# Performance work log

Measured on AMD Instinct MI355X. Metric: run time of the kernel, lower is better.

The kernel has to match this reference:

```python
import jax, jax.numpy as jnp
import numpy as np

H = 128
N_USER, N_PC, N_URL = 100000, 20000, 50000
E_UP, E_UU = 250000, 500000
NUM_LAYERS = 2


def _sage(x_src, x_dst, src_idx, dst_idx, n_dst, Wl, bl, Wr):
    # PyG SAGEConv (aggr='mean', root_weight=True, lin_r bias=False):
    # out = lin_l(mean_j x_src[j]) + lin_r(x_dst)
    msg = x_src[src_idx]                                   # [E, H] gather
    agg = jax.ops.segment_sum(msg, dst_idx, num_segments=n_dst)
    cnt = jax.ops.segment_sum(jnp.ones((src_idx.shape[0], 1), x_src.dtype),
                              dst_idx, num_segments=n_dst)
    mean = agg / jnp.maximum(cnt, 1.0)
    return mean @ Wl + bl + x_dst @ Wr


def setup_inputs() -> dict:
    key = jax.random.key(0)
    ks = jax.random.split(key, 24)
    s = 0.05
    inp = {
        'x_user': jax.random.normal(ks[0], (N_USER, 6), jnp.float32),
        'x_pc': jax.random.normal(ks[1], (N_PC, 4), jnp.float32),
        'x_url': jax.random.normal(ks[2], (N_URL, 3), jnp.float32),
        'edge_up_src': jax.random.randint(ks[3], (E_UP,), 0, N_USER, jnp.int32),
        'edge_up_dst': jax.random.randint(ks[4], (E_UP,), 0, N_PC, jnp.int32),
        'edge_uu_src': jax.random.randint(ks[5], (E_UU,), 0, N_USER, jnp.int32),
        'edge_uu_dst': jax.random.randint(ks[6], (E_UU,), 0, N_URL, jnp.int32),
        # input projections
        'Wu': jax.random.normal(ks[7], (6, H), jnp.float32) * s,
        'bu': jnp.zeros((H,), jnp.float32),
        'Wp': jax.random.normal(ks[8], (4, H), jnp.float32) * s,
        'bp': jnp.zeros((H,), jnp.float32),
        'Wr_feat': jax.random.normal(ks[9], (3, H), jnp.float32) * s,
        'br_feat': jnp.zeros((H,), jnp.float32),
        # SAGEConv params, stacked over layers [L, H, H]
        'Wl_pc': jax.random.normal(ks[10], (NUM_LAYERS, H, H), jnp.float32) * s,
        'bl_pc': jnp.zeros((NUM_LAYERS, H), jnp.float32),
        'Wr_pc': jax.random.normal(ks[11], (NUM_LAYERS, H, H), jnp.float32) * s,
        'Wl_url': jax.random.normal(ks[12], (NUM_LAYERS, H, H), jnp.float32) * s,
        'bl_url': jnp.zeros((NUM_LAYERS, H), jnp.float32),
        'Wr_url': jax.random.normal(ks[13], (NUM_LAYERS, H, H), jnp.float32) * s,
        # context aggregation + classifier
        'Wctx': jax.random.normal(ks[14], (3 * H, H), jnp.float32) * s,
        'bctx': jnp.zeros((H,), jnp.float32),
        'Wc1': jax.random.normal(ks[15], (H, H // 2), jnp.float32) * s,
        'bc1': jnp.zeros((H // 2,), jnp.float32),
        'Wc2': jax.random.normal(ks[16], (H // 2, 2), jnp.float32) * s,
        'bc2': jnp.zeros((2,), jnp.float32),
    }
    return inp


def reference(x_user, x_pc, x_url,
              edge_up_src, edge_up_dst, edge_uu_src, edge_uu_dst,
              Wu, bu, Wp, bp, Wr_feat, br_feat,
              Wl_pc, bl_pc, Wr_pc, Wl_url, bl_url, Wr_url,
              Wctx, bctx, Wc1, bc1, Wc2, bc2):
    user = x_user @ Wu + bu          # [N_USER, H] (never updated by convs)
    pc = x_pc @ Wp + bp              # [N_PC, H]
    url = x_url @ Wr_feat + br_feat  # [N_URL, H]

    for i in range(NUM_LAYERS):
        pc_new = _sage(user, pc, edge_up_src, edge_up_dst, pc.shape[0],
                       Wl_pc[i], bl_pc[i], Wr_pc[i])
        url_new = _sage(user, url, edge_uu_src, edge_uu_dst, url.shape[0],
                        Wl_url[i], bl_url[i], Wr_url[i])
        if i == 0:
            pc = jax.nn.relu(pc_new)
            url = jax.nn.relu(url_new)
        else:
            pc = jax.nn.relu(pc_new + pc)
            url = jax.nn.relu(url_new + url)

    # aggregate_resource_context: scatter-add of resource embeddings into users
    pc_ctx = jax.ops.segment_sum(pc[edge_up_dst], edge_up_src, num_segments=user.shape[0])
    url_ctx = jax.ops.segment_sum(url[edge_uu_dst], edge_uu_src, num_segments=user.shape[0])
    combined = jnp.concatenate([user, pc_ctx, url_ctx], axis=1)   # [N_USER, 3H]
    enriched = combined @ Wctx + bctx

    # classifier (dropout inactive at inference)
    h = jax.nn.relu(enriched @ Wc1 + bc1)
    return h @ Wc2 + bc2
```

## Files before the change

kernel.cpp:

```cpp
#include <hip/hip_runtime.h>

typedef unsigned short u16;
typedef short short8_t __attribute__((ext_vector_type(8)));
typedef float floatx4 __attribute__((ext_vector_type(4)));

static constexpr int N_USER_C = 100000;
static constexpr int N_PC_C   = 20000;
static constexpr int N_URL_C  = 50000;
static constexpr int E_UP_C   = 250000;
static constexpr int E_UU_C   = 500000;

static constexpr int S_UPD = 48;
static constexpr int S_UUD = 40;
static constexpr int S_SRC = 24;

__device__ __forceinline__ float bf2f(u16 h) {
    return __uint_as_float(((unsigned)h) << 16);
}
__device__ __forceinline__ u16 f2bf(float f) {
    unsigned u = __float_as_uint(f);
    u += 0x7fffu + ((u >> 16) & 1u);
    return (u16)(u >> 16);
}

struct WcvtArgs { const float* src[12]; int n[12]; };

__global__ __launch_bounds__(256) void wcvt_kernel(WcvtArgs args, u16* __restrict__ dst)
{
    int idx = blockIdx.x * 256 + threadIdx.x;
    int m = idx >> 14, e = idx & 16383;
    int n = e >> 7, k = e & 127;
    int Nm = args.n[m];
    u16 v = 0;
    if (n < Nm) v = f2bf(args.src[m][k * Nm + n]);
    dst[(size_t)m * 16384 + n * 128 + k] = v;
}

struct Proj3Args {
    const float *Xu, *Wu, *bu, *Xp, *Wp, *bp, *Xr, *Wr, *br;
    u16 *ou, *op, *orr;
};
__global__ __launch_bounds__(256) void proj3_kernel(Proj3Args a)
{
    int idx = blockIdx.x * 256 + threadIdx.x;
    const float* X; const float* W; const float* b; u16* o; int K;
    if (idx < 1600000)       { X = a.Xu; W = a.Wu; b = a.bu; o = a.ou; K = 6; }
    else if (idx < 1920000)  { idx -= 1600000; X = a.Xp; W = a.Wp; b = a.bp; o = a.op; K = 4; }
    else                     { idx -= 1920000; X = a.Xr; W = a.Wr; b = a.br; o = a.orr; K = 3; }
    int r = idx >> 4, c0 = (idx & 15) * 8;
    float acc[8];
    {
        const float4 b0 = *(const float4*)(b + c0);
        const float4 b1 = *(const float4*)(b + c0 + 4);
        acc[0] = b0.x; acc[1] = b0.y; acc[2] = b0.z; acc[3] = b0.w;
        acc[4] = b1.x; acc[5] = b1.y; acc[6] = b1.z; acc[7] = b1.w;
    }
    for (int k = 0; k < K; ++k) {
        float xk = X[(size_t)r * K + k];
        const float4 w0 = *(const float4*)(W + k * 128 + c0);
        const float4 w1 = *(const float4*)(W + k * 128 + c0 + 4);
        acc[0] += xk * w0.x; acc[1] += xk * w0.y; acc[2] += xk * w0.z; acc[3] += xk * w0.w;
        acc[4] += xk * w1.x; acc[5] += xk * w1.y; acc[6] += xk * w1.z; acc[7] += xk * w1.w;
    }
    uint4 pk;
    pk.x = (unsigned)f2bf(acc[0]) | ((unsigned)f2bf(acc[1]) << 16);
    pk.y = (unsigned)f2bf(acc[2]) | ((unsigned)f2bf(acc[3]) << 16);
    pk.z = (unsigned)f2bf(acc[4]) | ((unsigned)f2bf(acc[5]) << 16);
    pk.w = (unsigned)f2bf(acc[6]) | ((unsigned)f2bf(acc[7]) << 16);
    *(uint4*)(o + (size_t)r * 128 + c0) = pk;
}

__global__ __launch_bounds__(256) void fill_all_kernel(
    const int* __restrict__ up_src, const int* __restrict__ up_dst,
    const int* __restrict__ uu_src, const int* __restrict__ uu_dst,
    int* __restrict__ cnt_up_dst, int* __restrict__ val_up_dst,
    int* __restrict__ cnt_up_src, u16* __restrict__ val_up_src,
    int* __restrict__ cnt_uu_dst, int* __restrict__ val_uu_dst,
    int* __restrict__ cnt_uu_src, u16* __restrict__ val_uu_src)
{
    const int range = blockIdx.x & 7;
    const int ebase = (blockIdx.x >> 3) * 2048 + threadIdx.x;
#pragma unroll
    for (int i = 0; i < 8; ++i) {
        int e = ebase + i * 256;
        if (e < E_UP_C) {
            int s = up_src[e], d = up_dst[e];
            if (d / 2500 == range) {
                int p = atomicAdd(&cnt_up_dst[d], 1);
                if (p < S_UPD) val_up_dst[d * S_UPD + p] = s;
            }
            if (s / 12500 == range) {
                int p = atomicAdd(&cnt_up_src[s], 1);
                if (p < S_SRC) val_up_src[s * S_SRC + p] = (u16)d;
            }
        }
        if (e < E_UU_C) {
            int s = uu_src[e], d = uu_dst[e];
            if (d / 6250 == range) {
                int p = atomicAdd(&cnt_uu_dst[d], 1);
                if (p < S_UUD) val_uu_dst[d * S_UUD + p] = s;
            }
            if (s / 12500 == range) {
                int p = atomicAdd(&cnt_uu_src[s], 1);
                if (p < S_SRC) val_uu_src[s * S_SRC + p] = (u16)d;
            }
        }
    }
}

__device__ __forceinline__ void gm_row(
    const u16* __restrict__ feat, const int* __restrict__ cnt,
    const int* __restrict__ vals, int stride, u16* __restrict__ outp, int row, int lane)
{
    int deg = cnt[row];
    deg = __builtin_amdgcn_readfirstlane(deg);
    int n = deg < stride ? deg : stride;
    const int* vp = vals + row * stride;
    float a0 = 0.f, a1 = 0.f, b0 = 0.f, b1 = 0.f;
    float c0 = 0.f, c1 = 0.f, d0 = 0.f, d1 = 0.f;
    int j = 0;
    for (; j + 4 <= n; j += 4) {
        int i0 = vp[j], i1 = vp[j + 1], i2 = vp[j + 2], i3 = vp[j + 3];
        unsigned u0 = *(const unsigned*)(feat + (size_t)i0 * 128 + lane * 2);
        unsigned u1 = *(const unsigned*)(feat + (size_t)i1 * 128 + lane * 2);
        unsigned u2 = *(const unsigned*)(feat + (size_t)i2 * 128 + lane * 2);
        unsigned u3 = *(const unsigned*)(feat + (size_t)i3 * 128 + lane * 2);
        a0 += bf2f((u16)(u0 & 0xffff)); a1 += bf2f((u16)(u0 >> 16));
        b0 += bf2f((u16)(u1 & 0xffff)); b1 += bf2f((u16)(u1 >> 16));
        c0 += bf2f((u16)(u2 & 0xffff)); c1 += bf2f((u16)(u2 >> 16));
        d0 += bf2f((u16)(u3 & 0xffff)); d1 += bf2f((u16)(u3 >> 16));
    }
    for (; j < n; ++j) {
        int i0 = vp[j];
        unsigned u0 = *(const unsigned*)(feat + (size_t)i0 * 128 + lane * 2);
        a0 += bf2f((u16)(u0 & 0xffff)); a1 += bf2f((u16)(u0 >> 16));
    }
    float ax = (a0 + b0) + (c0 + d0), ay = (a1 + b1) + (c1 + d1);
    float inv = 1.0f / fmaxf((float)deg, 1.0f);
    unsigned o = (unsigned)f2bf(ax * inv) | ((unsigned)f2bf(ay * inv) << 16);
    *(unsigned*)(outp + (size_t)row * 128 + lane * 2) = o;
}

__global__ __launch_bounds__(256) void gather_mean2_kernel(
    const u16* __restrict__ feat,
    const int* __restrict__ cnt_pc, const int* __restrict__ val_pc, u16* __restrict__ out_pc,
    const int* __restrict__ cnt_url, const int* __restrict__ val_url, u16* __restrict__ out_url)
{
    int b = blockIdx.x;
    int lane = threadIdx.x & 63, w = threadIdx.x >> 6;
    if (b < 5000) gm_row(feat, cnt_pc, val_pc, S_UPD, out_pc, b * 4 + w, lane);
    else          gm_row(feat, cnt_url, val_url, S_UUD, out_url, (b - 5000) * 4 + w, lane);
}

__device__ __forceinline__ unsigned ctx_ld(int t, int n0, const u16* __restrict__ vu,
    const u16* __restrict__ vr,
    const u16* __restrict__ pcW, const u16* __restrict__ urlW, int lane)
{
    bool isup = t < n0;
    const u16* vp = isup ? (vu + t) : (vr + (t - n0));
    int idx = *vp;
    const u16* base = isup ? pcW : urlW;
    return *(const unsigned*)(base + (size_t)idx * 128 + lane * 2);
}

__global__ __launch_bounds__(256) void ctx_gather_kernel(
    u16* __restrict__ enr,
    const int* __restrict__ cnt_up, const u16* __restrict__ val_up, const u16* __restrict__ pcW,
    const int* __restrict__ cnt_uu, const u16* __restrict__ val_uu, const u16* __restrict__ urlW,
    int M)
{
    int row = blockIdx.x * 4 + (threadIdx.x >> 6);
    if (row >= M) return;
    int lane = threadIdx.x & 63;
    int n0 = cnt_up[row], n1 = cnt_uu[row];
    n0 = __builtin_amdgcn_readfirstlane(n0); n1 = __builtin_amdgcn_readfirstlane(n1);
    n0 = n0 < S_SRC ? n0 : S_SRC; n1 = n1 < S_SRC ? n1 : S_SRC;
    int total = n0 + n1;
    const u16* vu = val_up + row * S_SRC;
    const u16* vr = val_uu + row * S_SRC;

    unsigned eu = *(const unsigned*)(enr + (size_t)row * 128 + lane * 2);
    float a0 = bf2f((u16)(eu & 0xffff)), a1 = bf2f((u16)(eu >> 16));
    float b0 = 0.f, b1 = 0.f, c0 = 0.f, c1 = 0.f, d0 = 0.f, d1 = 0.f;

    int t = 0;
    for (; t + 4 <= total; t += 4) {
        unsigned u0 = ctx_ld(t + 0, n0, vu, vr, pcW, urlW, lane);
        unsigned u1 = ctx_ld(t + 1, n0, vu, vr, pcW, urlW, lane);
        unsigned u2 = ctx_ld(t + 2, n0, vu, vr, pcW, urlW, lane);
        unsigned u3 = ctx_ld(t + 3, n0, vu, vr, pcW, urlW, lane);
        a0 += bf2f((u16)(u0 & 0xffff)); a1 += bf2f((u16)(u0 >> 16));
        b0 += bf2f((u16)(u1 & 0xffff)); b1 += bf2f((u16)(u1 >> 16));
        c0 += bf2f((u16)(u2 & 0xffff)); c1 += bf2f((u16)(u2 >> 16));
        d0 += bf2f((u16)(u3 & 0xffff)); d1 += bf2f((u16)(u3 >> 16));
    }
    for (; t < total; ++t) {
        unsigned u0 = ctx_ld(t, n0, vu, vr, pcW, urlW, lane);
        a0 += bf2f((u16)(u0 & 0xffff)); a1 += bf2f((u16)(u0 >> 16));
    }
    float ax = (a0 + b0) + (c0 + d0), ay = (a1 + b1) + (c1 + d1);
    unsigned o = (unsigned)f2bf(ax) | ((unsigned)f2bf(ay) << 16);
    *(unsigned*)(enr + (size_t)row * 128 + lane * 2) = o;
}

struct GSeg { const u16* A1; const u16* Wt1; const u16* A2; const u16* Wt2;
              const float* bias; u16* out; int M; int bstart; };
template<int NSEG> struct GArgs { GSeg s[NSEG]; };

template<int NT, bool HAS2, bool RES, bool RELU, int NSEG>
__global__ __launch_bounds__(256) void gemm_multi_kernel(GArgs<NSEG> ga)
{
    constexpr int ROWS = NT * 16;
    constexpr int PER_ROW = 256 / ROWS;
    constexpr int CHUNK = 32 / PER_ROW;
    constexpr int NC = HAS2 ? 8 : 4;

    __shared__ u16 Ws[ROWS * 40];

    int si = 0;
#pragma unroll
    for (int i = 1; i < NSEG; ++i) if ((int)blockIdx.x >= ga.s[i].bstart) si = i;
    const u16* A1 = ga.s[si].A1;  const u16* Wt1 = ga.s[si].Wt1;
    const u16* A2 = ga.s[si].A2;  const u16* Wt2 = ga.s[si].Wt2;
    const float* bias = ga.s[si].bias;
    u16* out = ga.s[si].out;
    const int M = ga.s[si].M;
    const int bb = blockIdx.x - ga.s[si].bstart;

    const int tid = threadIdx.x;
    const int wave = tid >> 6, lane = tid & 63;
    const int m = lane & 15, kq = lane >> 4;
    const int rbase = bb * 128 + wave * 32;
    const int sn = tid / PER_ROW, spart = tid % PER_ROW;

    floatx4 acc[2][NT];
#pragma unroll
    for (int mt = 0; mt < 2; ++mt)
#pragma unroll
        for (int nt = 0; nt < NT; ++nt) acc[mt][nt] = (floatx4)0.0f;

    short8_t a_next[2];
#pragma unroll
    for (int mt = 0; mt < 2; ++mt) {
        int row = rbase + mt * 16 + m; row = row < M ? row : M - 1;
        a_next[mt] = *(const short8_t*)(A1 + (size_t)row * 128 + kq * 8);
    }

    for (int c = 0; c < NC; ++c) {
        const int kc = (HAS2 ? (c & 3) : c) * 32;
        const u16* Wt = (HAS2 && (c >> 2)) ? Wt2 : Wt1;
        __syncthreads();
#pragma unroll
        for (int j = 0; j < CHUNK / 8; ++j) {
            short8_t v = *(const short8_t*)(Wt + (size_t)sn * 128 + kc + spart * CHUNK + j * 8);
            *(short8_t*)&Ws[sn * 40 + spart * CHUNK + j * 8] = v;
        }
        short8_t a_cur[2] = { a_next[0], a_next[1] };
        __syncthreads();
        if (c + 1 < NC) {
            int c1 = c + 1;
            int kc1 = (HAS2 ? (c1 & 3) : c1) * 32;
            const u16* Ap = (HAS2 && (c1 >> 2)) ? A2 : A1;
#pragma unroll
            for (int mt = 0; mt < 2; ++mt) {
                int row = rbase + mt * 16 + m; row = row < M ? row : M - 1;
                a_next[mt] = *(const short8_t*)(Ap + (size_t)row * 128 + kc1 + kq * 8);
            }
        }
#pragma unroll
        for (int nt = 0; nt < NT; ++nt) {
            short8_t b = *(const short8_t*)&Ws[(nt * 16 + m) * 40 + kq * 8];
            acc[0][nt] = __builtin_amdgcn_mfma_f32_16x16x32_bf16(a_cur[0], b, acc[0][nt], 0, 0, 0);
            acc[1][nt] = __builtin_amdgcn_mfma_f32_16x16x32_bf16(a_cur[1], b, acc[1][nt], 0, 0, 0);
        }
    }

#pragma unroll
    for (int nt = 0; nt < NT; ++nt) {
        int col = nt * 16 + m;
        float bv = bias ? bias[col] : 0.0f;
#pragma unroll
        for (int mt = 0; mt < 2; ++mt) {
#pragma unroll
            for (int r = 0; r < 4; ++r) {
                int row = rbase + mt * 16 + kq * 4 + r;
                if (row < M) {
                    float v = acc[mt][nt][r] + bv;
                    if (RES) v += bf2f(A2[(size_t)row * 128 + col]);
                    if (RELU) v = fmaxf(v, 0.f);
                    out[(size_t)row * ROWS + col] = f2bf(v);
                }
            }
        }
    }
}

__global__ __launch_bounds__(256) void gemm_final_kernel(
    const u16* __restrict__ A1, const u16* __restrict__ Wt1,
    const float* __restrict__ bc1, const float* __restrict__ Wc2,
    const float* __restrict__ bc2, float* __restrict__ out, int M)
{
    constexpr int NT = 4;
    constexpr int PER_ROW = 4;
    constexpr int CHUNK = 8;
    constexpr int NC = 4;

    __shared__ u16 Ws[64 * 40];

    const int tid = threadIdx.x;
    const int wave = tid >> 6, lane = tid & 63;
    const int m = lane & 15, kq = lane >> 4;
    const int rbase = blockIdx.x * 128 + wave * 32;
    const int sn = tid / PER_ROW, spart = tid % PER_ROW;

    floatx4 acc[2][NT];
#pragma unroll
    for (int mt = 0; mt < 2; ++mt)
#pragma unroll
        for (int nt = 0; nt < NT; ++nt) acc[mt][nt] = (floatx4)0.0f;

    short8_t a_next[2];
#pragma unroll
    for (int mt = 0; mt < 2; ++mt) {
        int row = rbase + mt * 16 + m; row = row < M ? row : M - 1;
        a_next[mt] = *(const short8_t*)(A1 + (size_t)row * 128 + kq * 8);
    }

    for (int c = 0; c < NC; ++c) {
        const int kc = c * 32;
        __syncthreads();
        {
            short8_t v = *(const short8_t*)(Wt1 + (size_t)sn * 128 + kc + spart * CHUNK);
            *(short8_t*)&Ws[sn * 40 + spart * CHUNK] = v;
        }
        short8_t a_cur[2] = { a_next[0], a_next[1] };
        __syncthreads();
        if (c + 1 < NC) {
            int kc1 = (c + 1) * 32;
#pragma unroll
            for (int mt = 0; mt < 2; ++mt) {
                int row = rbase + mt * 16 + m; row = row < M ? row : M - 1;
                a_next[mt] = *(const short8_t*)(A1 + (size_t)row * 128 + kc1 + kq * 8);
            }
        }
#pragma unroll
        for (int nt = 0; nt < NT; ++nt) {
            short8_t b = *(const short8_t*)&Ws[(nt * 16 + m) * 40 + kq * 8];
            acc[0][nt] = __builtin_amdgcn_mfma_f32_16x16x32_bf16(a_cur[0], b, acc[0][nt], 0, 0, 0);
            acc[1][nt] = __builtin_amdgcn_mfma_f32_16x16x32_bf16(a_cur[1], b, acc[1][nt], 0, 0, 0);
        }
    }

    float w0v[NT], w1v[NT], bv[NT];
#pragma unroll
    for (int nt = 0; nt < NT; ++nt) {
        int col = nt * 16 + m;
        w0v[nt] = Wc2[col * 2 + 0];
        w1v[nt] = Wc2[col * 2 + 1];
        bv[nt]  = bc1[col];
    }
    float b20 = bc2[0], b21 = bc2[1];

#pragma unroll
    for (int mt = 0; mt < 2; ++mt) {
#pragma unroll
        for (int r = 0; r < 4; ++r) {
            float o0 = 0.f, o1 = 0.f;
#pragma unroll
            for (int nt = 0; nt < NT; ++nt) {
                float v = acc[mt][nt][r] + bv[nt];
                v = fmaxf(v, 0.f);
                o0 += v * w0v[nt];
                o1 += v * w1v[nt];
            }
#pragma unroll
            for (int off = 1; off < 16; off <<= 1) {
                o0 += __shfl_xor(o0, off, 64);
                o1 += __shfl_xor(o1, off, 64);
            }
            if (m == 0) {
                int row = rbase + mt * 16 + kq * 4 + r;
                if (row < M) {
                    out[(size_t)row * 2 + 0] = o0 + b20;
                    out[(size_t)row * 2 + 1] = o1 + b21;
                }
            }
        }
    }
}

extern "C" void kernel_launch(void* const* d_in, const int* in_sizes, int n_in,
                              void* d_out, int out_size, void* d_ws, size_t ws_size,
                              hipStream_t stream)
{
    const float* x_user  = (const float*)d_in[0];
    const float* x_pc    = (const float*)d_in[1];
    const float* x_url   = (const float*)d_in[2];
    const int* e_up_src  = (const int*)d_in[3];
    const int* e_up_dst  = (const int*)d_in[4];
    const int* e_uu_src  = (const int*)d_in[5];
    const int* e_uu_dst  = (const int*)d_in[6];
    const float* Wu      = (const float*)d_in[7];
    const float* bu      = (const float*)d_in[8];
    const float* Wp      = (const float*)d_in[9];
    const float* bp      = (const float*)d_in[10];
    const float* Wr_feat = (const float*)d_in[11];
    const float* br_feat = (const float*)d_in[12];
    const float* Wl_pc   = (const float*)d_in[13];
    const float* bl_pc   = (const float*)d_in[14];
    const float* Wr_pc   = (const float*)d_in[15];
    const float* Wl_url  = (const float*)d_in[16];
    const float* bl_url  = (const float*)d_in[17];
    const float* Wr_url  = (const float*)d_in[18];
    const float* Wctx    = (const float*)d_in[19];
    const float* bctx    = (const float*)d_in[20];
    const float* Wc1     = (const float*)d_in[21];
    const float* bc1     = (const float*)d_in[22];
    const float* Wc2     = (const float*)d_in[23];
    const float* bc2     = (const float*)d_in[24];
    float* out = (float*)d_out;

    char* wsb = (char*)d_ws;
    u16* user_bf  = (u16*)(wsb);
    u16* enr      = (u16*)(wsb + 4ull *  6400000);
    u16* mean_pc  = (u16*)(wsb + 4ull * 12800000);
    u16* mean_url = (u16*)(wsb + 4ull * 14080000);
    u16* pc_a     = (u16*)(wsb + 4ull * 17280000);
    u16* pc_b     = (u16*)(wsb + 4ull * 18560000);
    u16* url_a    = (u16*)(wsb + 4ull * 19840000);
    u16* url_b    = (u16*)(wsb + 4ull * 23040000);
    u16* Wt       = (u16*)(wsb + 4ull * 26240000);
    int* cnts     = (int*)(wsb + 4ull * 26340000);
    int* up_dst_val = (int*)(wsb + 4ull * 26610000);
    int* uu_dst_val = (int*)(wsb + 4ull * 27570000);
    u16* up_src_val = (u16*)(wsb + 4ull * 29570000);
    u16* uu_src_val = (u16*)(wsb + 4ull * 30770000);

    int* cnt_up_dst = cnts + 0;
    int* cnt_uu_dst = cnts + 20000;
    int* cnt_up_src = cnts + 70000;
    int* cnt_uu_src = cnts + 170000;

    const int T = 256;

    WcvtArgs wa;
    wa.src[0] = Wl_pc;               wa.src[1] = Wr_pc;
    wa.src[2] = Wl_pc + 128 * 128;   wa.src[3] = Wr_pc + 128 * 128;
    wa.src[4] = Wl_url;              wa.src[5] = Wr_url;
    wa.src[6] = Wl_url + 128 * 128;  wa.src[7] = Wr_url + 128 * 128;
    wa.src[8] = Wctx;                wa.src[9] = Wctx + 128 * 128;
    wa.src[10] = Wctx + 256 * 128;   wa.src[11] = Wc1;
    for (int i = 0; i < 12; ++i) wa.n[i] = 128;
    wa.n[11] = 64;
    wcvt_kernel<<<768, T, 0, stream>>>(wa, Wt);

    Proj3Args pa;
    pa.Xu = x_user; pa.Wu = Wu;      pa.bu = bu;      pa.ou = user_bf;
    pa.Xp = x_pc;   pa.Wp = Wp;      pa.bp = bp;      pa.op = pc_a;
    pa.Xr = x_url;  pa.Wr = Wr_feat; pa.br = br_feat; pa.orr = url_a;
    proj3_kernel<<<10625, T, 0, stream>>>(pa);

    hipMemsetAsync(cnts, 0, 270000ull * 4, stream);
    fill_all_kernel<<<245 * 8, T, 0, stream>>>(
        e_up_src, e_up_dst, e_uu_src, e_uu_dst,
        cnt_up_dst, up_dst_val, cnt_up_src, up_src_val,
        cnt_uu_dst, uu_dst_val, cnt_uu_src, uu_src_val);

    gather_mean2_kernel<<<5000 + 12500, T, 0, stream>>>(
        user_bf, cnt_up_dst, up_dst_val, mean_pc, cnt_uu_dst, uu_dst_val, mean_url);

    {
        GArgs<2> g;
        g.s[0] = { mean_pc,  Wt + 0 * 16384, pc_a,  Wt + 1 * 16384, bl_pc,  pc_b,  N_PC_C,  0 };
        g.s[1] = { mean_url, Wt + 4 * 16384, url_a, Wt + 5 * 16384, bl_url, url_b, N_URL_C, 157 };
        gemm_multi_kernel<8, true, false, true, 2><<<548, T, 0, stream>>>(g);
    }
    {
        GArgs<2> g;
        g.s[0] = { mean_pc,  Wt + 2 * 16384, pc_b,  Wt + 3 * 16384, bl_pc + 128,  pc_a,  N_PC_C,  0 };
        g.s[1] = { mean_url, Wt + 6 * 16384, url_b, Wt + 7 * 16384, bl_url + 128, url_a, N_URL_C, 157 };
        gemm_multi_kernel<8, true, true, true, 2><<<548, T, 0, stream>>>(g);
    }
    {
        GArgs<3> g;
        g.s[0] = { user_bf, Wt + 8 * 16384,  nullptr, nullptr, bctx,    enr,   N_USER_C, 0 };
        g.s[1] = { pc_a,    Wt + 9 * 16384,  nullptr, nullptr, nullptr, pc_b,  N_PC_C,   782 };
        g.s[2] = { url_a,   Wt + 10 * 16384, nullptr, nullptr, nullptr, url_b, N_URL_C,  939 };
        gemm_multi_kernel<8, false, false, false, 3><<<1330, T, 0, stream>>>(g);
    }

    ctx_gather_kernel<<<(N_USER_C + 3) / 4, T, 0, stream>>>(
        enr, cnt_up_src, up_src_val, pc_b, cnt_uu_src, uu_src_val, url_b, N_USER_C);

    gemm_final_kernel<<<(N_USER_C + 127) / 128, T, 0, stream>>>(
        enr, Wt + 11 * 16384, bc1, Wc2, bc2, out, N_USER_C);
}
```

Baseline: 372.9 us.

## Fuse SAGE layers and context projection into one LDS-resident GEMM kernel

The three GEMM launches (layer 1, layer 2 and the context projection) become one kernel. Each 128-row tile of pc/url runs both SAGE layers and the Wctx projection, keeping intermediate activations in LDS instead of writing them to global memory and reading them back. The weight conversion, input projection and counter memset are merged into a single prep kernel, and index loads use nontemporal hints. In exchange, the fused kernel uses more LDS, which may lower occupancy, and it drops the software prefetch of A tiles, which may expose load latency.

```diff
diff --git a/kernel.cpp b/kernel.cpp
--- a/kernel.cpp
+++ b/kernel.cpp
@@ -23,51 +23,55 @@
     return (u16)(u >> 16);
 }
 
-struct WcvtArgs { const float* src[12]; int n[12]; };
-
-__global__ __launch_bounds__(256) void wcvt_kernel(WcvtArgs args, u16* __restrict__ dst)
-{
-    int idx = blockIdx.x * 256 + threadIdx.x;
-    int m = idx >> 14, e = idx & 16383;
-    int n = e >> 7, k = e & 127;
-    int Nm = args.n[m];
-    u16 v = 0;
-    if (n < Nm) v = f2bf(args.src[m][k * Nm + n]);
-    dst[(size_t)m * 16384 + n * 128 + k] = v;
-}
-
-struct Proj3Args {
+struct PrepArgs {
+    const float* wsrc[12];
+    u16* wdst;
     const float *Xu, *Wu, *bu, *Xp, *Wp, *bp, *Xr, *Wr, *br;
     u16 *ou, *op, *orr;
+    int* cnts;
 };
-__global__ __launch_bounds__(256) void proj3_kernel(Proj3Args a)
-{
-    int idx = blockIdx.x * 256 + threadIdx.x;
-    const float* X; const float* W; const float* b; u16* o; int K;
-    if (idx < 1600000)       { X = a.Xu; W = a.Wu; b = a.bu; o = a.ou; K = 6; }
-    else if (idx < 1920000)  { idx -= 1600000; X = a.Xp; W = a.Wp; b = a.bp; o = a.op; K = 4; }
-    else                     { idx -= 1920000; X = a.Xr; W = a.Wr; b = a.br; o = a.orr; K = 3; }
-    int r = idx >> 4, c0 = (idx & 15) * 8;
-    float acc[8];
-    {
-        const float4 b0 = *(const float4*)(b + c0);
-        const float4 b1 = *(const float4*)(b + c0 + 4);
-        acc[0] = b0.x; acc[1] = b0.y; acc[2] = b0.z; acc[3] = b0.w;
-        acc[4] = b1.x; acc[5] = b1.y; acc[6] = b1.z; acc[7] = b1.w;
-    }
-    for (int k = 0; k < K; ++k) {
-        float xk = X[(size_t)r * K + k];
-        const float4 w0 = *(const float4*)(W + k * 128 + c0);
-        const float4 w1 = *(const float4*)(W + k * 128 + c0 + 4);
-        acc[0] += xk * w0.x; acc[1] += xk * w0.y; acc[2] += xk * w0.z; acc[3] += xk * w0.w;
-        acc[4] += xk * w1.x; acc[5] += xk * w1.y; acc[6] += xk * w1.z; acc[7] += xk * w1.w;
-    }
-    uint4 pk;
-    pk.x = (unsigned)f2bf(acc[0]) | ((unsigned)f2bf(acc[1]) << 16);
-    pk.y = (unsigned)f2bf(acc[2]) | ((unsigned)f2bf(acc[3]) << 16);
-    pk.z = (unsigned)f2bf(acc[4]) | ((unsigned)f2bf(acc[5]) << 16);
-    pk.w = (unsigned)f2bf(acc[6]) | ((unsigned)f2bf(acc[7]) << 16);
-    *(uint4*)(o + (size_t)r * 128 + c0) = pk;
+__global__ __launch_bounds__(256) void prep_kernel(PrepArgs a)
+{
+    int b = blockIdx.x, tid = threadIdx.x;
+    if (b < 768) {
+        int idx = b * 256 + tid;
+        int m = idx >> 14, e = idx & 16383;
+        int n = e >> 7, k = e & 127;
+        int Nm = (m == 11) ? 64 : 128;
+        u16 v = 0;
+        if (n < Nm) v = f2bf(a.wsrc[m][k * Nm + n]);
+        a.wdst[(size_t)m * 16384 + n * 128 + k] = v;
+    } else if (b < 768 + 10625) {
+        int idx = (b - 768) * 256 + tid;
+        const float* X; const float* W; const float* bi; u16* o; int K;
+        if (idx < 1600000)       { X = a.Xu; W = a.Wu; bi = a.bu; o = a.ou; K = 6; }
+        else if (idx < 1920000)  { idx -= 1600000; X = a.Xp; W = a.Wp; bi = a.bp; o = a.op; K = 4; }
+        else                     { idx -= 1920000; X = a.Xr; W = a.Wr; bi = a.br; o = a.orr; K = 3; }
+        int r = idx >> 4, c0 = (idx & 15) * 8;
+        float acc[8];
+        {
+            const float4 b0 = *(const float4*)(bi + c0);
+            const float4 b1 = *(const float4*)(bi + c0 + 4);
+            acc[0] = b0.x; acc[1] = b0.y; acc[2] = b0.z; acc[3] = b0.w;
+            acc[4] = b1.x; acc[5] = b1.y; acc[6] = b1.z; acc[7] = b1.w;
+        }
+        for (int k = 0; k < K; ++k) {
+            float xk = X[(size_t)r * K + k];
+            const float4 w0 = *(const float4*)(W + k * 128 + c0);
+            const float4 w1 = *(const float4*)(W + k * 128 + c0 + 4);
+            acc[0] += xk * w0.x; acc[1] += xk * w0.y; acc[2] += xk * w0.z; acc[3] += xk * w0.w;
+            acc[4] += xk * w1.x; acc[5] += xk * w1.y; acc[6] += xk * w1.z; acc[7] += xk * w1.w;
+        }
+        uint4 pk;
+        pk.x = (unsigned)f2bf(acc[0]) | ((unsigned)f2bf(acc[1]) << 16);
+        pk.y = (unsigned)f2bf(acc[2]) | ((unsigned)f2bf(acc[3]) << 16);
+        pk.z = (unsigned)f2bf(acc[4]) | ((unsigned)f2bf(acc[5]) << 16);
+        pk.w = (unsigned)f2bf(acc[6]) | ((unsigned)f2bf(acc[7]) << 16);
+        *(uint4*)(o + (size_t)r * 128 + c0) = pk;
+    } else {
+        int i = ((b - 11393) * 256 + tid) * 4;
+        if (i < 270000) *(int4*)(a.cnts + i) = make_int4(0, 0, 0, 0);
+    }
 }
 
 __global__ __launch_bounds__(256) void fill_all_kernel(
@@ -84,7 +88,8 @@
     for (int i = 0; i < 8; ++i) {
         int e = ebase + i * 256;
         if (e < E_UP_C) {
-            int s = up_src[e], d = up_dst[e];
+            int s = __builtin_nontemporal_load(up_src + e);
+            int d = __builtin_nontemporal_load(up_dst + e);
             if (d / 2500 == range) {
                 int p = atomicAdd(&cnt_up_dst[d], 1);
                 if (p < S_UPD) val_up_dst[d * S_UPD + p] = s;
@@ -95,7 +100,8 @@
             }
         }
         if (e < E_UU_C) {
-            int s = uu_src[e], d = uu_dst[e];
+            int s = __builtin_nontemporal_load(uu_src + e);
+            int d = __builtin_nontemporal_load(uu_dst + e);
             if (d / 6250 == range) {
                 int p = atomicAdd(&cnt_uu_dst[d], 1);
                 if (p < S_UUD) val_uu_dst[d * S_UUD + p] = s;
@@ -120,7 +126,10 @@
     float c0 = 0.f, c1 = 0.f, d0 = 0.f, d1 = 0.f;
     int j = 0;
     for (; j + 4 <= n; j += 4) {
-        int i0 = vp[j], i1 = vp[j + 1], i2 = vp[j + 2], i3 = vp[j + 3];
+        int i0 = __builtin_nontemporal_load(vp + j);
+        int i1 = __builtin_nontemporal_load(vp + j + 1);
+        int i2 = __builtin_nontemporal_load(vp + j + 2);
+        int i3 = __builtin_nontemporal_load(vp + j + 3);
         unsigned u0 = *(const unsigned*)(feat + (size_t)i0 * 128 + lane * 2);
         unsigned u1 = *(const unsigned*)(feat + (size_t)i1 * 128 + lane * 2);
         unsigned u2 = *(const unsigned*)(feat + (size_t)i2 * 128 + lane * 2);
@@ -131,7 +140,7 @@
         d0 += bf2f((u16)(u3 & 0xffff)); d1 += bf2f((u16)(u3 >> 16));
     }
     for (; j < n; ++j) {
-        int i0 = vp[j];
+        int i0 = __builtin_nontemporal_load(vp + j);
         unsigned u0 = *(const unsigned*)(feat + (size_t)i0 * 128 + lane * 2);
         a0 += bf2f((u16)(u0 & 0xffff)); a1 += bf2f((u16)(u0 >> 16));
     }
@@ -158,7 +167,7 @@
 {
     bool isup = t < n0;
     const u16* vp = isup ? (vu + t) : (vr + (t - n0));
-    int idx = *vp;
+    int idx = __builtin_nontemporal_load(vp);
     const u16* base = isup ? pcW : urlW;
     return *(const unsigned*)(base + (size_t)idx * 128 + lane * 2);
 }
@@ -203,95 +212,131 @@
     *(unsigned*)(enr + (size_t)row * 128 + lane * 2) = o;
 }
 
-struct GSeg { const u16* A1; const u16* Wt1; const u16* A2; const u16* Wt2;
-              const float* bias; u16* out; int M; int bstart; };
-template<int NSEG> struct GArgs { GSeg s[NSEG]; };
-
-template<int NT, bool HAS2, bool RES, bool RELU, int NSEG>
-__global__ __launch_bounds__(256) void gemm_multi_kernel(GArgs<NSEG> ga)
-{
-    constexpr int ROWS = NT * 16;
-    constexpr int PER_ROW = 256 / ROWS;
-    constexpr int CHUNK = 32 / PER_ROW;
-    constexpr int NC = HAS2 ? 8 : 4;
-
-    __shared__ u16 Ws[ROWS * 40];
+struct FSeg {
+    const u16 *mean, *x0;
+    const u16 *Wl0, *Wr0, *Wl1, *Wr1, *Wc;
+    const float *b0, *b1;
+    u16* out; int M; int bstart; int mode;
+};
+struct FArgs { FSeg s[3]; };
+
+__global__ __launch_bounds__(256) void gemm_fused_kernel(FArgs fa)
+{
+    constexpr int XP = 136;
+    __shared__ u16 Ws[128 * 40];
+    __shared__ u16 Xs[128 * XP];
 
     int si = 0;
-#pragma unroll
-    for (int i = 1; i < NSEG; ++i) if ((int)blockIdx.x >= ga.s[i].bstart) si = i;
-    const u16* A1 = ga.s[si].A1;  const u16* Wt1 = ga.s[si].Wt1;
-    const u16* A2 = ga.s[si].A2;  const u16* Wt2 = ga.s[si].Wt2;
-    const float* bias = ga.s[si].bias;
-    u16* out = ga.s[si].out;
-    const int M = ga.s[si].M;
-    const int bb = blockIdx.x - ga.s[si].bstart;
+    if ((int)blockIdx.x >= fa.s[1].bstart) si = 1;
+    if ((int)blockIdx.x >= fa.s[2].bstart) si = 2;
+    FSeg sg = fa.s[si];
+    const int bb = blockIdx.x - sg.bstart;
 
     const int tid = threadIdx.x;
     const int wave = tid >> 6, lane = tid & 63;
     const int m = lane & 15, kq = lane >> 4;
-    const int rbase = bb * 128 + wave * 32;
-    const int sn = tid / PER_ROW, spart = tid % PER_ROW;
-
-    floatx4 acc[2][NT];
-#pragma unroll
-    for (int mt = 0; mt < 2; ++mt)
-#pragma unroll
-        for (int nt = 0; nt < NT; ++nt) acc[mt][nt] = (floatx4)0.0f;
-
-    short8_t a_next[2];
-#pragma unroll
-    for (int mt = 0; mt < 2; ++mt) {
-        int row = rbase + mt * 16 + m; row = row < M ? row : M - 1;
-        a_next[mt] = *(const short8_t*)(A1 + (size_t)row * 128 + kq * 8);
-    }
-
-    for (int c = 0; c < NC; ++c) {
-        const int kc = (HAS2 ? (c & 3) : c) * 32;
-        const u16* Wt = (HAS2 && (c >> 2)) ? Wt2 : Wt1;
-        __syncthreads();
-#pragma unroll
-        for (int j = 0; j < CHUNK / 8; ++j) {
-            short8_t v = *(const short8_t*)(Wt + (size_t)sn * 128 + kc + spart * CHUNK + j * 8);
-            *(short8_t*)&Ws[sn * 40 + spart * CHUNK + j * 8] = v;
-        }
-        short8_t a_cur[2] = { a_next[0], a_next[1] };
-        __syncthreads();
-        if (c + 1 < NC) {
-            int c1 = c + 1;
-            int kc1 = (HAS2 ? (c1 & 3) : c1) * 32;
-            const u16* Ap = (HAS2 && (c1 >> 2)) ? A2 : A1;
-#pragma unroll
-            for (int mt = 0; mt < 2; ++mt) {
-                int row = rbase + mt * 16 + m; row = row < M ? row : M - 1;
-                a_next[mt] = *(const short8_t*)(Ap + (size_t)row * 128 + kc1 + kq * 8);
-            }
-        }
-#pragma unroll
-        for (int nt = 0; nt < NT; ++nt) {
+    const int rloc = wave * 32;
+    const int rbase = bb * 128 + rloc;
+    const int sn = tid >> 1, spart = tid & 1;
+
+    floatx4 acc[2][8];
+
+    auto zeroAcc = [&]() {
+#pragma unroll
+        for (int mt = 0; mt < 2; ++mt)
+#pragma unroll
+            for (int nt = 0; nt < 8; ++nt) acc[mt][nt] = (floatx4)0.0f;
+    };
+    auto stageW = [&](const u16* Wt, int kc) {
+        *(short8_t*)&Ws[sn * 40 + spart * 16] =
+            *(const short8_t*)(Wt + (size_t)sn * 128 + kc + spart * 16);
+        *(short8_t*)&Ws[sn * 40 + spart * 16 + 8] =
+            *(const short8_t*)(Wt + (size_t)sn * 128 + kc + spart * 16 + 8);
+    };
+    auto loadAg = [&](const u16* A, int kc, int mt) -> short8_t {
+        int row = rbase + mt * 16 + m; row = row < sg.M ? row : sg.M - 1;
+        return *(const short8_t*)(A + (size_t)row * 128 + kc + kq * 8);
+    };
+    auto loadAs = [&](int kc, int mt) -> short8_t {
+        return *(const short8_t*)&Xs[(rloc + mt * 16 + m) * XP + kc + kq * 8];
+    };
+    auto mfmaChunk = [&](short8_t a0, short8_t a1) {
+#pragma unroll
+        for (int nt = 0; nt < 8; ++nt) {
             short8_t b = *(const short8_t*)&Ws[(nt * 16 + m) * 40 + kq * 8];
-            acc[0][nt] = __builtin_amdgcn_mfma_f32_16x16x32_bf16(a_cur[0], b, acc[0][nt], 0, 0, 0);
-            acc[1][nt] = __builtin_amdgcn_mfma_f32_16x16x32_bf16(a_cur[1], b, acc[1][nt], 0, 0, 0);
-        }
-    }
-
-#pragma unroll
-    for (int nt = 0; nt < NT; ++nt) {
-        int col = nt * 16 + m;
-        float bv = bias ? bias[col] : 0.0f;
-#pragma unroll
-        for (int mt = 0; mt < 2; ++mt) {
-#pragma unroll
-            for (int r = 0; r < 4; ++r) {
-                int row = rbase + mt * 16 + kq * 4 + r;
-                if (row < M) {
+            acc[0][nt] = __builtin_amdgcn_mfma_f32_16x16x32_bf16(a0, b, acc[0][nt], 0, 0, 0);
+            acc[1][nt] = __builtin_amdgcn_mfma_f32_16x16x32_bf16(a1, b, acc[1][nt], 0, 0, 0);
+        }
+    };
+    auto passDual = [&](const u16* W1, const u16* A1g, const u16* W2, const u16* A2g, bool a2lds) {
+        zeroAcc();
+        for (int c = 0; c < 8; ++c) {
+            int kc = (c & 3) * 32;
+            const u16* Wt = (c < 4) ? W1 : W2;
+            __syncthreads();
+            stageW(Wt, kc);
+            __syncthreads();
+            short8_t a0, a1;
+            if (c < 4)      { a0 = loadAg(A1g, kc, 0); a1 = loadAg(A1g, kc, 1); }
+            else if (a2lds) { a0 = loadAs(kc, 0);      a1 = loadAs(kc, 1); }
+            else            { a0 = loadAg(A2g, kc, 0); a1 = loadAg(A2g, kc, 1); }
+            mfmaChunk(a0, a1);
+        }
+    };
+    auto passSingle = [&](const u16* W1, const u16* A1g, bool lds) {
+        zeroAcc();
+        for (int c = 0; c < 4; ++c) {
+            int kc = c * 32;
+            __syncthreads();
+            stageW(W1, kc);
+            __syncthreads();
+            short8_t a0, a1;
+            if (lds) { a0 = loadAs(kc, 0); a1 = loadAs(kc, 1); }
+            else     { a0 = loadAg(A1g, kc, 0); a1 = loadAg(A1g, kc, 1); }
+            mfmaChunk(a0, a1);
+        }
+    };
+    auto epilogueToLds = [&](const float* bias, bool addRes) {
+#pragma unroll
+        for (int nt = 0; nt < 8; ++nt) {
+            int col = nt * 16 + m;
+            float bv = bias[col];
+#pragma unroll
+            for (int mt = 0; mt < 2; ++mt)
+#pragma unroll
+                for (int r = 0; r < 4; ++r) {
+                    int lrow = rloc + mt * 16 + kq * 4 + r;
                     float v = acc[mt][nt][r] + bv;
-                    if (RES) v += bf2f(A2[(size_t)row * 128 + col]);
-                    if (RELU) v = fmaxf(v, 0.f);
-                    out[(size_t)row * ROWS + col] = f2bf(v);
+                    if (addRes) v += bf2f(Xs[lrow * XP + col]);
+                    Xs[lrow * XP + col] = f2bf(fmaxf(v, 0.f));
                 }
-            }
-        }
+        }
+    };
+    auto epilogueToGlobal = [&](const float* bias, u16* outp) {
+#pragma unroll
+        for (int nt = 0; nt < 8; ++nt) {
+            int col = nt * 16 + m;
+            float bv = bias ? bias[col] : 0.0f;
+#pragma unroll
+            for (int mt = 0; mt < 2; ++mt)
+#pragma unroll
+                for (int r = 0; r < 4; ++r) {
+                    int row = rbase + mt * 16 + kq * 4 + r;
+                    if (row < sg.M) outp[(size_t)row * 128 + col] = f2bf(acc[mt][nt][r] + bv);
+                }
+        }
+    };
+
+    if (sg.mode == 0) {
+        passDual(sg.Wl0, sg.mean, sg.Wr0, sg.x0, false);
+        epilogueToLds(sg.b0, false);
+        passDual(sg.Wl1, sg.mean, sg.Wr1, nullptr, true);
+        epilogueToLds(sg.b1, true);
+        passSingle(sg.Wc, nullptr, true);
+        epilogueToGlobal(nullptr, sg.out);
+    } else {
+        passSingle(sg.Wl0, sg.mean, false);
+        epilogueToGlobal(sg.b0, sg.out);
     }
 }
 
@@ -327,10 +372,9 @@
     }
 
     for (int c = 0; c < NC; ++c) {
-        const int kc = c * 32;
         __syncthreads();
         {
-            short8_t v = *(const short8_t*)(Wt1 + (size_t)sn * 128 + kc + spart * CHUNK);
+            short8_t v = *(const short8_t*)(Wt1 + (size_t)sn * 128 + c * 32 + spart * CHUNK);
             *(short8_t*)&Ws[sn * 40 + spart * CHUNK] = v;
         }
         short8_t a_cur[2] = { a_next[0], a_next[1] };
@@ -443,24 +487,20 @@
 
     const int T = 256;
 
-    WcvtArgs wa;
-    wa.src[0] = Wl_pc;               wa.src[1] = Wr_pc;
-    wa.src[2] = Wl_pc + 128 * 128;   wa.src[3] = Wr_pc + 128 * 128;
-    wa.src[4] = Wl_url;              wa.src[5] = Wr_url;
-    wa.src[6] = Wl_url + 128 * 128;  wa.src[7] = Wr_url + 128 * 128;
-    wa.src[8] = Wctx;                wa.src[9] = Wctx + 128 * 128;
-    wa.src[10] = Wctx + 256 * 128;   wa.src[11] = Wc1;
-    for (int i = 0; i < 12; ++i) wa.n[i] = 128;
-    wa.n[11] = 64;
-    wcvt_kernel<<<768, T, 0, stream>>>(wa, Wt);
-
-    Proj3Args pa;
+    PrepArgs pa;
+    pa.wsrc[0] = Wl_pc;               pa.wsrc[1] = Wr_pc;
+    pa.wsrc[2] = Wl_pc + 128 * 128;   pa.wsrc[3] = Wr_pc + 128 * 128;
+    pa.wsrc[4] = Wl_url;              pa.wsrc[5] = Wr_url;
+    pa.wsrc[6] = Wl_url + 128 * 128;  pa.wsrc[7] = Wr_url + 128 * 128;
+    pa.wsrc[8] = Wctx;                pa.wsrc[9] = Wctx + 128 * 128;
+    pa.wsrc[10] = Wctx + 256 * 128;   pa.wsrc[11] = Wc1;
+    pa.wdst = Wt;
     pa.Xu = x_user; pa.Wu = Wu;      pa.bu = bu;      pa.ou = user_bf;
     pa.Xp = x_pc;   pa.Wp = Wp;      pa.bp = bp;      pa.op = pc_a;
     pa.Xr = x_url;  pa.Wr = Wr_feat; pa.br = br_feat; pa.orr = url_a;
-    proj3_kernel<<<10625, T, 0, stream>>>(pa);
-
-    hipMemsetAsync(cnts, 0, 270000ull * 4, stream);
+    pa.cnts = cnts;
+    prep_kernel<<<768 + 10625 + 264, T, 0, stream>>>(pa);
+
     fill_all_kernel<<<245 * 8, T, 0, stream>>>(
         e_up_src, e_up_dst, e_uu_src, e_uu_dst,
         cnt_up_dst, up_dst_val, cnt_up_src, up_src_val,
@@ -469,25 +509,14 @@
     gather_mean2_kernel<<<5000 + 12500, T, 0, stream>>>(
         user_bf, cnt_up_dst, up_dst_val, mean_pc, cnt_uu_dst, uu_dst_val, mean_url);
 
-    {
-        GArgs<2> g;
-        g.s[0] = { mean_pc,  Wt + 0 * 16384, pc_a,  Wt + 1 * 16384, bl_pc,  pc_b,  N_PC_C,  0 };
-        g.s[1] = { mean_url, Wt + 4 * 16384, url_a, Wt + 5 * 16384, bl_url, url_b, N_URL_C, 157 };
-        gemm_multi_kernel<8, true, false, true, 2><<<548, T, 0, stream>>>(g);
-    }
-    {
-        GArgs<2> g;
-        g.s[0] = { mean_pc,  Wt + 2 * 16384, pc_b,  Wt + 3 * 16384, bl_pc + 128,  pc_a,  N_PC_C,  0 };
-        g.s[1] = { mean_url, Wt + 6 * 16384, url_b, Wt + 7 * 16384, bl_url + 128, url_a, N_URL_C, 157 };
-        gemm_multi_kernel<8, true, true, true, 2><<<548, T, 0, stream>>>(g);
-    }
-    {
-        GArgs<3> g;
-        g.s[0] = { user_bf, Wt + 8 * 16384,  nullptr, nullptr, bctx,    enr,   N_USER_C, 0 };
-        g.s[1] = { pc_a,    Wt + 9 * 16384,  nullptr, nullptr, nullptr, pc_b,  N_PC_C,   782 };
-        g.s[2] = { url_a,   Wt + 10 * 16384, nullptr, nullptr, nullptr, url_b, N_URL_C,  939 };
-        gemm_multi_kernel<8, false, false, false, 3><<<1330, T, 0, stream>>>(g);
-    }
+    FArgs fg;
+    fg.s[0] = { mean_pc,  pc_a,  Wt + 0 * 16384, Wt + 1 * 16384, Wt + 2 * 16384, Wt + 3 * 16384,
+                Wt + 9 * 16384,  bl_pc,  bl_pc + 128,  pc_b,  N_PC_C,   0,   0 };
+    fg.s[1] = { mean_url, url_a, Wt + 4 * 16384, Wt + 5 * 16384, Wt + 6 * 16384, Wt + 7 * 16384,
+                Wt + 10 * 16384, bl_url, bl_url + 128, url_b, N_URL_C,  157, 0 };
+    fg.s[2] = { user_bf,  nullptr, Wt + 8 * 16384, nullptr, nullptr, nullptr,
+                nullptr,         bctx,   nullptr,      enr,   N_USER_C, 548, 1 };
+    gemm_fused_kernel<<<548 + 782, T, 0, stream>>>(fg);
 
     ctx_gather_kernel<<<(N_USER_C + 3) / 4, T, 0, stream>>>(
         enr, cnt_up_src, up_src_val, pc_b, cnt_uu_src, uu_src_val, url_b, N_USER_C);
```

Result: faster. 359.5 us (-3.6%).
